# Optimization experiments

Hardware: AMD Instinct MI355X
Metric: run time of the kernel (lower is better)

Reference implementation:

```python
import jax, jax.numpy as jnp
import numpy as np

D = 512
VOCAB = 8192
UTT_LEN = 16
BATCH = 32
NTYPES = 8
MPT = 32
NLAYERS = 2


def setup_inputs() -> dict:
    key = jax.random.key(0)
    ks = jax.random.split(key, 16)
    d, dff, v1 = D, 4 * D, VOCAB + 1
    s = 0.02
    nrm = lambda k, shape: jax.random.normal(k, shape, dtype=jnp.float32) * s
    zeros = lambda shape: jnp.zeros(shape, jnp.float32)
    ones = lambda shape: jnp.ones(shape, jnp.float32)
    return {
        'meanings': jax.random.randint(ks[0], (BATCH, NTYPES), 0, MPT),
        'emb_table': nrm(ks[1], (NTYPES * MPT, d)),
        'v2e_w': nrm(ks[2], (v1, d)),
        'e2v_w': nrm(ks[3], (v1, d)),
        'e2v_b': zeros((v1,)),
        'sa_qkv_w': nrm(ks[4], (NLAYERS, 3 * d, d)),
        'sa_qkv_b': zeros((NLAYERS, 3 * d)),
        'sa_out_w': nrm(ks[5], (NLAYERS, d, d)),
        'sa_out_b': zeros((NLAYERS, d)),
        'ca_qkv_w': nrm(ks[6], (NLAYERS, 3 * d, d)),
        'ca_qkv_b': zeros((NLAYERS, 3 * d)),
        'ca_out_w': nrm(ks[7], (NLAYERS, d, d)),
        'ca_out_b': zeros((NLAYERS, d)),
        'ffn_w1': nrm(ks[8], (NLAYERS, dff, d)),
        'ffn_b1': zeros((NLAYERS, dff)),
        'ffn_w2': nrm(ks[9], (NLAYERS, d, dff)),
        'ffn_b2': zeros((NLAYERS, d)),
        'ln1_g': ones((NLAYERS, d)), 'ln1_b': zeros((NLAYERS, d)),
        'ln2_g': ones((NLAYERS, d)), 'ln2_b': zeros((NLAYERS, d)),
        'ln3_g': ones((NLAYERS, d)), 'ln3_b': zeros((NLAYERS, d)),
    }


def _ln(x, g, b, eps=1e-5):
    m = x.mean(-1, keepdims=True)
    v = ((x - m) ** 2).mean(-1, keepdims=True)
    return (x - m) / jnp.sqrt(v + eps) * g + b


def _attn(q_in, kv_in, qkv_w, qkv_b, out_w, out_b, mask):
    # single-head attention, torch MultiheadAttention layout (seq, batch, d)
    d = q_in.shape[-1]
    q = q_in @ qkv_w[:d].T + qkv_b[:d]
    k = kv_in @ qkv_w[d:2 * d].T + qkv_b[d:2 * d]
    v = kv_in @ qkv_w[2 * d:].T + qkv_b[2 * d:]
    scores = jnp.einsum('qbd,kbd->bqk', q, k) / jnp.sqrt(jnp.float32(d))
    if mask is not None:
        scores = scores + mask
    a = jax.nn.softmax(scores, axis=-1)
    o = jnp.einsum('bqk,kbd->qbd', a, v)
    return o @ out_w.T + out_b


def _sinusoidal_pe(L, d):
    pos = np.arange(L)[:, None].astype(np.float32)
    div = np.exp(np.arange(0, d, 2).astype(np.float32) * (-np.log(10000.0) / d))
    pe = np.zeros((L, d), np.float32)
    pe[:, 0::2] = np.sin(pos * div)
    pe[:, 1::2] = np.cos(pos * div)
    return jnp.asarray(pe)[:, None, :]  # [L,1,d]


def reference(meanings, emb_table, v2e_w, e2v_w, e2v_b,
              sa_qkv_w, sa_qkv_b, sa_out_w, sa_out_b,
              ca_qkv_w, ca_qkv_b, ca_out_w, ca_out_b,
              ffn_w1, ffn_b1, ffn_w2, ffn_b2,
              ln1_g, ln1_b, ln2_g, ln2_b, ln3_g, ln3_b):
    B, T = meanings.shape
    v1, d = v2e_w.shape
    start_token = v1 - 1
    mpt = emb_table.shape[0] // T
    offs = jnp.arange(T, dtype=meanings.dtype) * mpt
    src = emb_table[meanings + offs].sum(axis=1)[None]  # [1,B,d] cross-attn memory
    L = UTT_LEN
    pe = _sinusoidal_pe(L, d)
    causal = jnp.where(jnp.tril(jnp.ones((L, L), bool)), 0.0, -jnp.inf).astype(jnp.float32)
    nlayers = sa_qkv_w.shape[0]

    def step(buf, i):
        # full-length decode with causal mask == original growing-prefix decode at position i
        x = v2e_w[buf[:L]] + pe  # [L,B,d]
        for l in range(nlayers):
            sa = _attn(x, x, sa_qkv_w[l], sa_qkv_b[l], sa_out_w[l], sa_out_b[l], causal)
            x = _ln(x + sa, ln1_g[l], ln1_b[l])
            ca = _attn(x, src, ca_qkv_w[l], ca_qkv_b[l], ca_out_w[l], ca_out_b[l], None)
            x = _ln(x + ca, ln2_g[l], ln2_b[l])
            ff = jax.nn.relu(x @ ffn_w1[l].T + ffn_b1[l]) @ ffn_w2[l].T + ffn_b2[l]
            x = _ln(x + ff, ln3_g[l], ln3_b[l])
        h = jnp.take(x, i, axis=0)         # [B,d] last generated position
        logits = h @ e2v_w.T + e2v_b        # [B,V+1]
        tok = jnp.argmax(logits, axis=-1).astype(buf.dtype)
        buf = buf.at[i + 1].set(tok)
        return buf, (tok, logits)

    buf0 = jnp.zeros((L + 1, B), jnp.int32).at[0].set(start_token)
    _, (toks, logits) = jax.lax.scan(step, buf0, jnp.arange(L))
    return toks, logits  # utterances [utt_len,B], per-step logits [utt_len,B,V+1]
```

## Files before the change

kernel.cpp:

```cpp
#include <hip/hip_runtime.h>
#include <cmath>

namespace {

constexpr int Dm  = 512;
constexpr int Bn  = 32;
constexpr int Lq  = 16;
constexpr int V1  = 8193;
constexpr int DFF = 2048;
constexpr int NL  = 2;
constexpr int NT  = 256;

__device__ __forceinline__ float wred(float v) {
#pragma unroll
  for (int off = 32; off; off >>= 1) v += __shfl_down(v, off, 64);
  return v;
}

__device__ __forceinline__ float dot4(const float4 w, const float4 x, float a) {
  a = fmaf(w.x, x.x, a); a = fmaf(w.y, x.y, a);
  a = fmaf(w.z, x.z, a); a = fmaf(w.w, x.w, a);
  return a;
}

__device__ __forceinline__ float pe_val(int pos, int t) {
  const int j2 = (t >> 1) << 1;
  const float div = expf((float)j2 * (-9.210340371976184f / 512.0f));
  const float ang = (float)pos * div;
  return (t & 1) ? cosf(ang) : sinf(ang);
}

template <int KS, int Kc, int SP, bool RELU>
__global__ __launch_bounds__(NT) void fg_part(
    const float* __restrict__ xsrc, int xstride, int srcPartStride,
    const float* __restrict__ W, int K,
    const float* __restrict__ bias,
    float* __restrict__ part, int N) {
  constexpr int QR = Kc / 4;
  __shared__ float smem[32 * Kc];
  const int kc = (int)blockIdx.x % KS;
  const int k0 = kc * Kc;
  for (int idx = threadIdx.x; idx < 8 * Kc; idx += NT) {
    const int b = idx / QR, q = idx - b * QR;
    const float* s0 = xsrc + (size_t)b * xstride + k0 + (q << 2);
    float4 v = *(const float4*)(s0);
#pragma unroll
    for (int s = 1; s < SP; ++s) {
      const float4 u = *(const float4*)(s0 + (size_t)s * srcPartStride);
      v.x += u.x; v.y += u.y; v.z += u.z; v.w += u.w;
    }
    if (RELU) {
      v.x = fmaxf(v.x, 0.f); v.y = fmaxf(v.y, 0.f);
      v.z = fmaxf(v.z, 0.f); v.w = fmaxf(v.w, 0.f);
    }
    *(float4*)(smem + b * Kc + ((q ^ (b & 7)) << 2)) = v;
  }
  __syncthreads();
  const int lane = (int)threadIdx.x & 63, wave = (int)threadIdx.x >> 6;
  const int bl = lane & 31, nh = lane >> 5, sw = bl & 7;
  const int rowjob = ((int)blockIdx.x / KS) * 4 + wave;
  const int n0 = (rowjob << 3) + (nh << 2);
  const float* xb = smem + bl * Kc;
  const float* w = W + (size_t)n0 * K + k0;
  float a0 = 0.f, a1 = 0.f, a2 = 0.f, a3 = 0.f;
#pragma unroll 4
  for (int qq = 0; qq < QR; ++qq) {
    const float4 xv = *(const float4*)(xb + ((qq ^ sw) << 2));
    const float* wq = w + (qq << 2);
    a0 = dot4(*(const float4*)(wq), xv, a0);
    a1 = dot4(*(const float4*)(wq + K), xv, a1);
    a2 = dot4(*(const float4*)(wq + 2 * K), xv, a2);
    a3 = dot4(*(const float4*)(wq + 3 * K), xv, a3);
  }
  if (kc == 0) {
    a0 += bias[n0]; a1 += bias[n0 + 1]; a2 += bias[n0 + 2]; a3 += bias[n0 + 3];
  }
  float* yb = part + (size_t)kc * 32 * N + (size_t)bl * N + n0;
  yb[0] = a0; yb[1] = a1; yb[2] = a2; yb[3] = a3;
}

__global__ __launch_bounds__(NT) void fg_qkv_part(const float* __restrict__ x,
    const float* __restrict__ W, const float* __restrict__ bias,
    float* __restrict__ qkvp) {
  constexpr int Kc = 128, QR = 32;
  __shared__ float smem[32 * Kc];
  const int kc = (int)blockIdx.x & 3;
  const int k0 = kc * Kc;
  for (int idx = threadIdx.x; idx < 8 * Kc; idx += NT) {
    const int b = idx / QR, q = idx - b * QR;
    const float4 v = *(const float4*)(x + (b << 9) + k0 + (q << 2));
    *(float4*)(smem + b * Kc + ((q ^ (b & 7)) << 2)) = v;
  }
  __syncthreads();
  const int lane = (int)threadIdx.x & 63, wave = (int)threadIdx.x >> 6;
  const int bl = lane & 31, nh = lane >> 5, sw = bl & 7;
  const int rowjob = ((int)blockIdx.x >> 2) * 4 + wave;
  const int n0 = (rowjob << 3) + (nh << 2);
  const float* xb = smem + bl * Kc;
  const float* w = W + (size_t)n0 * Dm + k0;
  float a0 = 0.f, a1 = 0.f, a2 = 0.f, a3 = 0.f;
#pragma unroll 4
  for (int qq = 0; qq < QR; ++qq) {
    const float4 xv = *(const float4*)(xb + ((qq ^ sw) << 2));
    const float* wq = w + (qq << 2);
    a0 = dot4(*(const float4*)(wq), xv, a0);
    a1 = dot4(*(const float4*)(wq + Dm), xv, a1);
    a2 = dot4(*(const float4*)(wq + 2 * Dm), xv, a2);
    a3 = dot4(*(const float4*)(wq + 3 * Dm), xv, a3);
  }
  if (kc == 0) {
    a0 += bias[n0]; a1 += bias[n0 + 1]; a2 += bias[n0 + 2]; a3 += bias[n0 + 3];
  }
  const int seg = n0 >> 9;
  float* yb = qkvp + (size_t)seg * 65536 + (size_t)kc * 16384 + (bl << 9) + (n0 & 511);
  yb[0] = a0; yb[1] = a1; yb[2] = a2; yb[3] = a3;
}

__device__ __forceinline__ void block_ln(float* s, const float* __restrict__ g,
                                         const float* __restrict__ bb, float* red) {
  const int tid = (int)threadIdx.x;
  float ls = 0.f, lq = 0.f;
  for (int t = tid; t < Dm; t += NT) { const float v = s[t]; ls += v; lq += v * v; }
  ls = wred(ls); lq = wred(lq);
  const int wave = tid >> 6, lane = tid & 63;
  if (lane == 0) { red[wave] = ls; red[4 + wave] = lq; }
  __syncthreads();
  const float sum = red[0] + red[1] + red[2] + red[3];
  const float sq  = red[4] + red[5] + red[6] + red[7];
  const float mean = sum * (1.f / Dm);
  const float var  = sq * (1.f / Dm) - mean * mean;
  const float inv  = 1.f / sqrtf(var + 1e-5f);
  __syncthreads();
  for (int t = tid; t < Dm; t += NT) s[t] = (s[t] - mean) * inv * g[t] + bb[t];
}

__global__ __launch_bounds__(NT) void attn_core(const float* __restrict__ qkvp,
    float* __restrict__ kcl, float* __restrict__ vcl,
    float* __restrict__ aout, int pos) {
  __shared__ float sQ[Dm], sK[Dm], sV[Dm], sS[Lq];
  const int b = blockIdx.x, tid = threadIdx.x, lane = tid & 63, wave = tid >> 6;
  const float* qp = qkvp;
  const float* kp = qkvp + 65536;
  const float* vp = qkvp + 131072;
  for (int t = tid; t < Dm; t += NT) {
    const int o = (b << 9) + t;
    const float qv = qp[o] + qp[o + 16384] + qp[o + 32768] + qp[o + 49152];
    const float kv = kp[o] + kp[o + 16384] + kp[o + 32768] + kp[o + 49152];
    const float vv = vp[o] + vp[o + 16384] + vp[o + 32768] + vp[o + 49152];
    sQ[t] = qv; sK[t] = kv; sV[t] = vv;
    const int co = ((pos * Bn + b) << 9) + t;
    kcl[co] = kv; vcl[co] = vv;
  }
  __syncthreads();
  for (int j = wave; j <= pos; j += 4) {
    float acc;
    if (j == pos) {
      acc = dot4(*(const float4*)(sK + (lane << 2)),
                 *(const float4*)(sQ + (lane << 2)), 0.f);
      acc = dot4(*(const float4*)(sK + 256 + (lane << 2)),
                 *(const float4*)(sQ + 256 + (lane << 2)), acc);
    } else {
      const float* kr = kcl + ((size_t)(j * Bn + b) << 9);
      acc = dot4(*(const float4*)(kr + (lane << 2)),
                 *(const float4*)(sQ + (lane << 2)), 0.f);
      acc = dot4(*(const float4*)(kr + 256 + (lane << 2)),
                 *(const float4*)(sQ + 256 + (lane << 2)), acc);
    }
    acc = wred(acc);
    if (lane == 0) sS[j] = acc * 0.044194173824159216f;
  }
  __syncthreads();
  if (tid == 0) {
    float m = -1e30f;
    for (int j = 0; j <= pos; ++j) m = fmaxf(m, sS[j]);
    float s = 0.f;
    for (int j = 0; j <= pos; ++j) { const float e = expf(sS[j] - m); sS[j] = e; s += e; }
    const float inv = 1.f / s;
    for (int j = 0; j <= pos; ++j) sS[j] *= inv;
  }
  __syncthreads();
  for (int t = tid; t < Dm; t += NT) {
    float acc = sS[pos] * sV[t];
    for (int j = 0; j < pos; ++j) acc += sS[j] * vcl[((size_t)(j * Bn + b) << 9) + t];
    aout[(b << 9) + t] = acc;
  }
}

__global__ __launch_bounds__(NT) void ln12(const float* __restrict__ sop,
    const float* __restrict__ caCp,
    const float* __restrict__ g1, const float* __restrict__ b1,
    const float* __restrict__ g2, const float* __restrict__ b2,
    float* __restrict__ x) {
  __shared__ float sR[Dm], red[8];
  const int b = blockIdx.x, tid = threadIdx.x;
  for (int t = tid; t < Dm; t += NT) {
    const int o = (b << 9) + t;
    sR[t] = x[o] + sop[o] + sop[o + 16384] + sop[o + 32768] + sop[o + 49152];
  }
  __syncthreads();
  block_ln(sR, g1, b1, red);
  __syncthreads();
  for (int t = tid; t < Dm; t += NT) {
    const int o = (b << 9) + t;
    sR[t] += caCp[o] + caCp[o + 16384] + caCp[o + 32768] + caCp[o + 49152];
  }
  __syncthreads();
  block_ln(sR, g2, b2, red);
  __syncthreads();
  for (int t = tid; t < Dm; t += NT) x[(b << 9) + t] = sR[t];
}

__global__ __launch_bounds__(NT) void ln3red(const float* __restrict__ f2p,
    const float* __restrict__ g3, const float* __restrict__ bb3,
    float* __restrict__ x) {
  __shared__ float sR[Dm], red[8];
  const int b = blockIdx.x, tid = threadIdx.x;
  for (int t = tid; t < Dm; t += NT) {
    const int o = (b << 9) + t;
    float v = x[o];
#pragma unroll
    for (int kc = 0; kc < 8; ++kc) v += f2p[kc * 16384 + o];
    sR[t] = v;
  }
  __syncthreads();
  block_ln(sR, g3, bb3, red);
  __syncthreads();
  for (int t = tid; t < Dm; t += NT) x[(b << 9) + t] = sR[t];
}

__global__ __launch_bounds__(512) void src_kernel(const int* __restrict__ meanings,
                                                  const float* __restrict__ emb,
                                                  float* __restrict__ src) {
  const int b = blockIdx.x, t = threadIdx.x;
  float s = 0.f;
#pragma unroll
  for (int ty = 0; ty < 8; ++ty) {
    const int idx = meanings[b * 8 + ty] + ty * 32;
    s += emb[(size_t)idx * Dm + t];
  }
  src[b * Dm + t] = s;
}

__global__ __launch_bounds__(512) void embed0(const float* __restrict__ v2e,
                                              float* __restrict__ x) {
  const int b = blockIdx.x, t = threadIdx.x;
  x[(b << 9) + t] = v2e[(size_t)(V1 - 1) * Dm + t] + pe_val(0, t);
}

__global__ __launch_bounds__(NT) void argmax_embed(float* __restrict__ x,
    const float* __restrict__ e2v_w, const float* __restrict__ e2v_b,
    const float* __restrict__ v2e, const float* __restrict__ lp,
    float* __restrict__ outLogits, float* __restrict__ outToks, int i) {
  __shared__ float red[8];
  __shared__ float sv[NT];
  __shared__ int   si[NT];
  const int b = blockIdx.x, tid = threadIdx.x, lane = tid & 63, wave = tid >> 6;
  float ls = 0.f;
  for (int t = tid; t < Dm; t += NT) ls += x[(b << 9) + t] * e2v_w[(size_t)8192 * Dm + t];
  ls = wred(ls);
  if (lane == 0) red[wave] = ls;
  __syncthreads();
  float* row = outLogits + ((size_t)i * Bn + b) * V1;
  if (tid == 0) {
    const float lg = red[0] + red[1] + red[2] + red[3] + e2v_b[8192];
    row[8192] = lg;
    red[4] = lg;
  }
  __syncthreads();
  const float lg = red[4];
  float best = -1e30f; int bi = 0;
  for (int v = tid; v < 8192; v += NT) {
    const float val = lp[(b << 13) + v] + lp[262144 + (b << 13) + v];
    row[v] = val;
    if (val > best) { best = val; bi = v; }
  }
  sv[tid] = best; si[tid] = bi;
  __syncthreads();
  for (int off = 128; off; off >>= 1) {
    if (tid < off) {
      const float v2 = sv[tid + off]; const int i2 = si[tid + off];
      if (v2 > sv[tid] || (v2 == sv[tid] && i2 < si[tid])) { sv[tid] = v2; si[tid] = i2; }
    }
    __syncthreads();
  }
  if (tid == 0) {
    int tok = si[0];
    if (lg > sv[0]) tok = 8192;
    outToks[i * Bn + b] = (float)tok;
    si[0] = tok;
  }
  __syncthreads();
  const int tok = si[0];
  if (i + 1 < Lq) {
    for (int t = tid; t < Dm; t += NT)
      x[(b << 9) + t] = v2e[(size_t)tok * Dm + t] + pe_val(i + 1, t);
  }
}

}

extern "C" void kernel_launch(void* const* d_in, const int* in_sizes, int n_in,
                              void* d_out, int out_size, void* d_ws, size_t ws_size,
                              hipStream_t stream) {
  (void)in_sizes; (void)n_in; (void)out_size; (void)ws_size;
  const int*   meanings  = (const int*)d_in[0];
  const float* emb_table = (const float*)d_in[1];
  const float* v2e_w     = (const float*)d_in[2];
  const float* e2v_w     = (const float*)d_in[3];
  const float* e2v_b     = (const float*)d_in[4];
  const float* sa_qkv_w  = (const float*)d_in[5];
  const float* sa_qkv_b  = (const float*)d_in[6];
  const float* sa_out_w  = (const float*)d_in[7];
  const float* sa_out_b  = (const float*)d_in[8];
  const float* ca_qkv_w  = (const float*)d_in[9];
  const float* ca_qkv_b  = (const float*)d_in[10];
  const float* ca_out_w  = (const float*)d_in[11];
  const float* ca_out_b  = (const float*)d_in[12];
  const float* ffn_w1    = (const float*)d_in[13];
  const float* ffn_b1    = (const float*)d_in[14];
  const float* ffn_w2    = (const float*)d_in[15];
  const float* ffn_b2    = (const float*)d_in[16];
  const float* ln1_g     = (const float*)d_in[17];
  const float* ln1_b     = (const float*)d_in[18];
  const float* ln2_g     = (const float*)d_in[19];
  const float* ln2_b     = (const float*)d_in[20];
  const float* ln3_g     = (const float*)d_in[21];
  const float* ln3_b     = (const float*)d_in[22];

  float* out = (float*)d_out;
  float* outLogits = out + Lq * Bn;

  float* f = (float*)d_ws;
  float* src  = f;  f += 16384;
  float* x    = f;  f += 16384;
  float* aout = f;  f += 16384;
  float* caCp = f;  f += 131072;
  float* regA = f;  f += 655360;
  float* kcache = f; f += 524288;
  float* vcache = f;
  float* qkvp = regA;
  float* sop  = regA + 196608;
  float* h1p  = regA + 262144;
  float* f2p  = regA + 524288;
  float* lp   = regA;

  src_kernel<<<Bn, 512, 0, stream>>>(meanings, emb_table, src);

  for (int l = 0; l < NL; ++l) {
    fg_part<4, 128, 1, false><<<64, NT, 0, stream>>>(src, Dm, 0,
        ca_qkv_w + ((size_t)l * 3 + 2) * Dm * Dm, Dm,
        ca_qkv_b + l * 3 * Dm + 2 * Dm, sop, Dm);
    fg_part<4, 128, 4, false><<<64, NT, 0, stream>>>(sop, Dm, 16384,
        ca_out_w + (size_t)l * Dm * Dm, Dm,
        ca_out_b + l * Dm, caCp + (size_t)l * 65536, Dm);
  }

  embed0<<<Bn, 512, 0, stream>>>(v2e_w, x);

  for (int i = 0; i < Lq; ++i) {
    for (int l = 0; l < NL; ++l) {
      float* kcl = kcache + (size_t)l * Lq * Bn * Dm;
      float* vcl = vcache + (size_t)l * Lq * Bn * Dm;
      fg_qkv_part<<<192, NT, 0, stream>>>(x,
          sa_qkv_w + (size_t)l * 3 * Dm * Dm, sa_qkv_b + l * 3 * Dm, qkvp);
      attn_core<<<Bn, NT, 0, stream>>>(qkvp, kcl, vcl, aout, i);
      fg_part<4, 128, 1, false><<<64, NT, 0, stream>>>(aout, Dm, 0,
          sa_out_w + (size_t)l * Dm * Dm, Dm, sa_out_b + l * Dm, sop, Dm);
      ln12<<<Bn, NT, 0, stream>>>(sop, caCp + (size_t)l * 65536,
          ln1_g + l * Dm, ln1_b + l * Dm, ln2_g + l * Dm, ln2_b + l * Dm, x);
      fg_part<4, 128, 1, false><<<256, NT, 0, stream>>>(x, Dm, 0,
          ffn_w1 + (size_t)l * DFF * Dm, Dm, ffn_b1 + l * DFF, h1p, DFF);
      fg_part<8, 256, 4, true><<<128, NT, 0, stream>>>(h1p, DFF, 65536,
          ffn_w2 + (size_t)l * Dm * DFF, DFF, ffn_b2 + l * Dm, f2p, Dm);
      ln3red<<<Bn, NT, 0, stream>>>(f2p,
          ln3_g + l * Dm, ln3_b + l * Dm, x);
    }
    fg_part<2, 256, 1, false><<<512, NT, 0, stream>>>(x, Dm, 0,
        e2v_w, Dm, e2v_b, lp, 8192);
    argmax_embed<<<Bn, NT, 0, stream>>>(x, e2v_w, e2v_b, v2e_w,
        lp, outLogits, out, i);
  }
}
```

Measured before the change: 2.736 ms.

## Fuse decode-step kernels using atomic ticket counters and in-kernel grid waits

Merges the per-layer chain of GEMV, attention, layernorm and FFN kernels into three kernels per step (qkv+attention, post-attention+FFN, logits+argmax). Global atomic counters act as barriers: the last-arriving blocks take tickets to run the dependent reduction or attention stages, and other blocks spin-wait on counters between phases. The aim is to cut kernel launch count and launch gaps in a latency-bound decode loop. In exchange, global traffic now uses relaxed atomic loads and stores, which may be slower than plain vector loads. The spin waits also assume every block is co-resident on the GPU, which holds for grids of up to 256 blocks.

```diff
diff --git a/kernel.cpp b/kernel.cpp
--- a/kernel.cpp
+++ b/kernel.cpp
@@ -11,6 +11,27 @@
 constexpr int NL  = 2;
 constexpr int NT  = 256;
 
+__device__ __forceinline__ float g_ld(const float* p) {
+  return __hip_atomic_load(p, __ATOMIC_RELAXED, __HIP_MEMORY_SCOPE_AGENT);
+}
+__device__ __forceinline__ void g_st(float* p, float v) {
+  __hip_atomic_store(p, v, __ATOMIC_RELAXED, __HIP_MEMORY_SCOPE_AGENT);
+}
+__device__ __forceinline__ float2 g_ld2(const float* p) {
+  unsigned long long u = __hip_atomic_load((const unsigned long long*)p,
+      __ATOMIC_RELAXED, __HIP_MEMORY_SCOPE_AGENT);
+  float2 r;
+  r.x = __uint_as_float((unsigned)u);
+  r.y = __uint_as_float((unsigned)(u >> 32));
+  return r;
+}
+__device__ __forceinline__ void g_st2(float* p, float a, float b) {
+  unsigned long long u = (unsigned long long)__float_as_uint(a) |
+                         ((unsigned long long)__float_as_uint(b) << 32);
+  __hip_atomic_store((unsigned long long*)p, u, __ATOMIC_RELAXED,
+                     __HIP_MEMORY_SCOPE_AGENT);
+}
+
 __device__ __forceinline__ float wred(float v) {
 #pragma unroll
   for (int off = 32; off; off >>= 1) v += __shfl_down(v, off, 64);
@@ -30,37 +51,87 @@
   return (t & 1) ? cosf(ang) : sinf(ang);
 }
 
+__device__ __forceinline__ void wait_ctr(const unsigned* c, unsigned n) {
+  if (threadIdx.x == 0) {
+    while (__hip_atomic_load(c, __ATOMIC_RELAXED, __HIP_MEMORY_SCOPE_AGENT) < n)
+      __builtin_amdgcn_s_sleep(2);
+    asm volatile("" ::: "memory");
+  }
+  __syncthreads();
+}
+
+__device__ void block_ln(float* s, const float* __restrict__ g,
+                         const float* __restrict__ bb, float* red) {
+  const int tid = (int)threadIdx.x;
+  float ls = 0.f, lq = 0.f;
+  for (int t = tid; t < Dm; t += NT) { const float v = s[t]; ls += v; lq += v * v; }
+  ls = wred(ls); lq = wred(lq);
+  const int wave = tid >> 6, lane = tid & 63;
+  if (lane == 0) { red[wave] = ls; red[4 + wave] = lq; }
+  __syncthreads();
+  const float sum = red[0] + red[1] + red[2] + red[3];
+  const float sq  = red[4] + red[5] + red[6] + red[7];
+  const float mean = sum * (1.f / Dm);
+  const float var  = sq * (1.f / Dm) - mean * mean;
+  const float inv  = 1.f / sqrtf(var + 1e-5f);
+  __syncthreads();
+  for (int t = tid; t < Dm; t += NT) s[t] = (s[t] - mean) * inv * g[t] + bb[t];
+}
+
+__global__ __launch_bounds__(512) void init_bar(unsigned* bar) {
+  const int i = (int)blockIdx.x * 512 + (int)threadIdx.x;
+  __hip_atomic_store(bar + i, 0u, __ATOMIC_RELAXED, __HIP_MEMORY_SCOPE_AGENT);
+}
+
+__global__ __launch_bounds__(512) void src_kernel(const int* __restrict__ meanings,
+    const float* __restrict__ emb, float* __restrict__ src) {
+  const int b = (int)blockIdx.x, t = (int)threadIdx.x;
+  float s = 0.f;
+#pragma unroll
+  for (int ty = 0; ty < 8; ++ty) {
+    const int idx = meanings[b * 8 + ty] + ty * 32;
+    s += emb[(size_t)idx * Dm + t];
+  }
+  g_st(src + b * Dm + t, s);
+}
+
+__global__ __launch_bounds__(512) void embed0(const float* __restrict__ v2e,
+                                              float* __restrict__ x) {
+  const int b = (int)blockIdx.x, t = (int)threadIdx.x;
+  g_st(x + (b << 9) + t, v2e[(size_t)(V1 - 1) * Dm + t] + pe_val(0, t));
+}
+
 template <int KS, int Kc, int SP, bool RELU>
-__global__ __launch_bounds__(NT) void fg_part(
-    const float* __restrict__ xsrc, int xstride, int srcPartStride,
-    const float* __restrict__ W, int K,
-    const float* __restrict__ bias,
+__global__ __launch_bounds__(NT) void k_fg(const float* __restrict__ xsrc, int xstride,
+    int pstride, const float* __restrict__ W, int K, const float* __restrict__ bias,
     float* __restrict__ part, int N) {
   constexpr int QR = Kc / 4;
   __shared__ float smem[32 * Kc];
-  const int kc = (int)blockIdx.x % KS;
-  const int k0 = kc * Kc;
-  for (int idx = threadIdx.x; idx < 8 * Kc; idx += NT) {
+  const int bid = (int)blockIdx.x, tid = (int)threadIdx.x;
+  const int kc = bid % KS, k0 = kc * Kc;
+  for (int idx = tid; idx < 8 * Kc; idx += NT) {
     const int b = idx / QR, q = idx - b * QR;
     const float* s0 = xsrc + (size_t)b * xstride + k0 + (q << 2);
-    float4 v = *(const float4*)(s0);
+    float2 lo = g_ld2(s0), hi = g_ld2(s0 + 2);
 #pragma unroll
     for (int s = 1; s < SP; ++s) {
-      const float4 u = *(const float4*)(s0 + (size_t)s * srcPartStride);
-      v.x += u.x; v.y += u.y; v.z += u.z; v.w += u.w;
+      const float2 l2 = g_ld2(s0 + (size_t)s * pstride);
+      const float2 h2 = g_ld2(s0 + (size_t)s * pstride + 2);
+      lo.x += l2.x; lo.y += l2.y; hi.x += h2.x; hi.y += h2.y;
     }
     if (RELU) {
-      v.x = fmaxf(v.x, 0.f); v.y = fmaxf(v.y, 0.f);
-      v.z = fmaxf(v.z, 0.f); v.w = fmaxf(v.w, 0.f);
-    }
+      lo.x = fmaxf(lo.x, 0.f); lo.y = fmaxf(lo.y, 0.f);
+      hi.x = fmaxf(hi.x, 0.f); hi.y = fmaxf(hi.y, 0.f);
+    }
+    float4 v; v.x = lo.x; v.y = lo.y; v.z = hi.x; v.w = hi.y;
     *(float4*)(smem + b * Kc + ((q ^ (b & 7)) << 2)) = v;
   }
   __syncthreads();
-  const int lane = (int)threadIdx.x & 63, wave = (int)threadIdx.x >> 6;
+  const int lane = tid & 63, wave = tid >> 6;
   const int bl = lane & 31, nh = lane >> 5, sw = bl & 7;
-  const int rowjob = ((int)blockIdx.x / KS) * 4 + wave;
+  const float* xb = smem + bl * Kc;
+  const int rowjob = (bid / KS) * 4 + wave;
   const int n0 = (rowjob << 3) + (nh << 2);
-  const float* xb = smem + bl * Kc;
   const float* w = W + (size_t)n0 * K + k0;
   float a0 = 0.f, a1 = 0.f, a2 = 0.f, a3 = 0.f;
 #pragma unroll 4
@@ -76,77 +147,68 @@
     a0 += bias[n0]; a1 += bias[n0 + 1]; a2 += bias[n0 + 2]; a3 += bias[n0 + 3];
   }
   float* yb = part + (size_t)kc * 32 * N + (size_t)bl * N + n0;
-  yb[0] = a0; yb[1] = a1; yb[2] = a2; yb[3] = a3;
-}
-
-__global__ __launch_bounds__(NT) void fg_qkv_part(const float* __restrict__ x,
+  g_st2(yb, a0, a1); g_st2(yb + 2, a2, a3);
+}
+
+__global__ __launch_bounds__(NT) void k_qkv_attn(const float* __restrict__ x,
     const float* __restrict__ W, const float* __restrict__ bias,
-    float* __restrict__ qkvp) {
-  constexpr int Kc = 128, QR = 32;
-  __shared__ float smem[32 * Kc];
-  const int kc = (int)blockIdx.x & 3;
-  const int k0 = kc * Kc;
-  for (int idx = threadIdx.x; idx < 8 * Kc; idx += NT) {
-    const int b = idx / QR, q = idx - b * QR;
-    const float4 v = *(const float4*)(x + (b << 9) + k0 + (q << 2));
-    *(float4*)(smem + b * Kc + ((q ^ (b & 7)) << 2)) = v;
-  }
-  __syncthreads();
-  const int lane = (int)threadIdx.x & 63, wave = (int)threadIdx.x >> 6;
-  const int bl = lane & 31, nh = lane >> 5, sw = bl & 7;
-  const int rowjob = ((int)blockIdx.x >> 2) * 4 + wave;
-  const int n0 = (rowjob << 3) + (nh << 2);
-  const float* xb = smem + bl * Kc;
-  const float* w = W + (size_t)n0 * Dm + k0;
-  float a0 = 0.f, a1 = 0.f, a2 = 0.f, a3 = 0.f;
+    float* __restrict__ qkvp, float* __restrict__ kcl, float* __restrict__ vcl,
+    float* __restrict__ aout, unsigned* ctr, int pos) {
+  __shared__ float smem[4096];
+  __shared__ int tkt_s;
+  const int bid = (int)blockIdx.x, tid = (int)threadIdx.x;
+  const int lane = tid & 63, wave = tid >> 6;
+  {
+    constexpr int Kc = 128;
+    const int kc = bid & 3, k0 = kc << 7;
+    for (int idx = tid; idx < 1024; idx += NT) {
+      const int b = idx >> 5, q = idx & 31;
+      const float* s0 = x + (b << 9) + k0 + (q << 2);
+      const float2 lo = g_ld2(s0), hi = g_ld2(s0 + 2);
+      float4 v; v.x = lo.x; v.y = lo.y; v.z = hi.x; v.w = hi.y;
+      *(float4*)(smem + b * Kc + ((q ^ (b & 7)) << 2)) = v;
+    }
+    __syncthreads();
+    const int bl = lane & 31, nh = lane >> 5, sw = bl & 7;
+    const float* xb = smem + bl * Kc;
+    const int rowjob = (bid >> 2) * 4 + wave;
+    const int n0 = (rowjob << 3) + (nh << 2);
+    const float* w = W + (size_t)n0 * Dm + k0;
+    float a0 = 0.f, a1 = 0.f, a2 = 0.f, a3 = 0.f;
 #pragma unroll 4
-  for (int qq = 0; qq < QR; ++qq) {
-    const float4 xv = *(const float4*)(xb + ((qq ^ sw) << 2));
-    const float* wq = w + (qq << 2);
-    a0 = dot4(*(const float4*)(wq), xv, a0);
-    a1 = dot4(*(const float4*)(wq + Dm), xv, a1);
-    a2 = dot4(*(const float4*)(wq + 2 * Dm), xv, a2);
-    a3 = dot4(*(const float4*)(wq + 3 * Dm), xv, a3);
-  }
-  if (kc == 0) {
-    a0 += bias[n0]; a1 += bias[n0 + 1]; a2 += bias[n0 + 2]; a3 += bias[n0 + 3];
-  }
-  const int seg = n0 >> 9;
-  float* yb = qkvp + (size_t)seg * 65536 + (size_t)kc * 16384 + (bl << 9) + (n0 & 511);
-  yb[0] = a0; yb[1] = a1; yb[2] = a2; yb[3] = a3;
-}
-
-__device__ __forceinline__ void block_ln(float* s, const float* __restrict__ g,
-                                         const float* __restrict__ bb, float* red) {
-  const int tid = (int)threadIdx.x;
-  float ls = 0.f, lq = 0.f;
-  for (int t = tid; t < Dm; t += NT) { const float v = s[t]; ls += v; lq += v * v; }
-  ls = wred(ls); lq = wred(lq);
-  const int wave = tid >> 6, lane = tid & 63;
-  if (lane == 0) { red[wave] = ls; red[4 + wave] = lq; }
-  __syncthreads();
-  const float sum = red[0] + red[1] + red[2] + red[3];
-  const float sq  = red[4] + red[5] + red[6] + red[7];
-  const float mean = sum * (1.f / Dm);
-  const float var  = sq * (1.f / Dm) - mean * mean;
-  const float inv  = 1.f / sqrtf(var + 1e-5f);
-  __syncthreads();
-  for (int t = tid; t < Dm; t += NT) s[t] = (s[t] - mean) * inv * g[t] + bb[t];
-}
-
-__global__ __launch_bounds__(NT) void attn_core(const float* __restrict__ qkvp,
-    float* __restrict__ kcl, float* __restrict__ vcl,
-    float* __restrict__ aout, int pos) {
-  __shared__ float sQ[Dm], sK[Dm], sV[Dm], sS[Lq];
-  const int b = blockIdx.x, tid = threadIdx.x, lane = tid & 63, wave = tid >> 6;
+    for (int qq = 0; qq < 32; ++qq) {
+      const float4 xv = *(const float4*)(xb + ((qq ^ sw) << 2));
+      const float* wq = w + (qq << 2);
+      a0 = dot4(*(const float4*)(wq), xv, a0);
+      a1 = dot4(*(const float4*)(wq + Dm), xv, a1);
+      a2 = dot4(*(const float4*)(wq + 2 * Dm), xv, a2);
+      a3 = dot4(*(const float4*)(wq + 3 * Dm), xv, a3);
+    }
+    if (kc == 0) {
+      a0 += bias[n0]; a1 += bias[n0 + 1]; a2 += bias[n0 + 2]; a3 += bias[n0 + 3];
+    }
+    const int seg = n0 >> 9;
+    float* yb = qkvp + (size_t)seg * 65536 + (size_t)kc * 16384 + (bl << 9) + (n0 & 511);
+    g_st2(yb, a0, a1); g_st2(yb + 2, a2, a3);
+  }
+  __syncthreads();
+  if (tid == 0)
+    tkt_s = (int)__hip_atomic_fetch_add(ctr, 1u, __ATOMIC_RELEASE, __HIP_MEMORY_SCOPE_AGENT);
+  __syncthreads();
+  const int tkt = tkt_s;
+  if (tkt < 160) return;
+  const int b = tkt - 160;
+  wait_ctr(ctr, 192);
+  float* sQ = smem; float* sK = smem + 512; float* sV = smem + 1024;
+  float* sS = smem + 1536;
   const float* qp = qkvp;
   const float* kp = qkvp + 65536;
   const float* vp = qkvp + 131072;
   for (int t = tid; t < Dm; t += NT) {
     const int o = (b << 9) + t;
-    const float qv = qp[o] + qp[o + 16384] + qp[o + 32768] + qp[o + 49152];
-    const float kv = kp[o] + kp[o + 16384] + kp[o + 32768] + kp[o + 49152];
-    const float vv = vp[o] + vp[o + 16384] + vp[o + 32768] + vp[o + 49152];
+    const float qv = g_ld(qp + o) + g_ld(qp + o + 16384) + g_ld(qp + o + 32768) + g_ld(qp + o + 49152);
+    const float kv = g_ld(kp + o) + g_ld(kp + o + 16384) + g_ld(kp + o + 32768) + g_ld(kp + o + 49152);
+    const float vv = g_ld(vp + o) + g_ld(vp + o + 16384) + g_ld(vp + o + 32768) + g_ld(vp + o + 49152);
     sQ[t] = qv; sK[t] = kv; sV[t] = vv;
     const int co = ((pos * Bn + b) << 9) + t;
     kcl[co] = kv; vcl[co] = vv;
@@ -182,97 +244,266 @@
   for (int t = tid; t < Dm; t += NT) {
     float acc = sS[pos] * sV[t];
     for (int j = 0; j < pos; ++j) acc += sS[j] * vcl[((size_t)(j * Bn + b) << 9) + t];
-    aout[(b << 9) + t] = acc;
-  }
-}
-
-__global__ __launch_bounds__(NT) void ln12(const float* __restrict__ sop,
-    const float* __restrict__ caCp,
+    g_st(aout + (b << 9) + t, acc);
+  }
+}
+
+__global__ __launch_bounds__(NT) void k_post(
+    const float* __restrict__ aout, const float* __restrict__ caCp_l,
+    float* __restrict__ x,
+    const float* __restrict__ saW, const float* __restrict__ saB,
     const float* __restrict__ g1, const float* __restrict__ b1,
     const float* __restrict__ g2, const float* __restrict__ b2,
-    float* __restrict__ x) {
-  __shared__ float sR[Dm], red[8];
-  const int b = blockIdx.x, tid = threadIdx.x;
-  for (int t = tid; t < Dm; t += NT) {
-    const int o = (b << 9) + t;
-    sR[t] = x[o] + sop[o] + sop[o + 16384] + sop[o + 32768] + sop[o + 49152];
-  }
-  __syncthreads();
-  block_ln(sR, g1, b1, red);
-  __syncthreads();
-  for (int t = tid; t < Dm; t += NT) {
-    const int o = (b << 9) + t;
-    sR[t] += caCp[o] + caCp[o + 16384] + caCp[o + 32768] + caCp[o + 49152];
-  }
-  __syncthreads();
-  block_ln(sR, g2, b2, red);
-  __syncthreads();
-  for (int t = tid; t < Dm; t += NT) x[(b << 9) + t] = sR[t];
-}
-
-__global__ __launch_bounds__(NT) void ln3red(const float* __restrict__ f2p,
-    const float* __restrict__ g3, const float* __restrict__ bb3,
-    float* __restrict__ x) {
-  __shared__ float sR[Dm], red[8];
-  const int b = blockIdx.x, tid = threadIdx.x;
-  for (int t = tid; t < Dm; t += NT) {
-    const int o = (b << 9) + t;
-    float v = x[o];
+    const float* __restrict__ f1W, const float* __restrict__ f1b,
+    const float* __restrict__ f2W, const float* __restrict__ f2b,
+    const float* __restrict__ g3, const float* __restrict__ b3,
+    float* __restrict__ sop, float* __restrict__ h1p, float* __restrict__ f2p,
+    unsigned* ctr) {
+  __shared__ float smem[8192];
+  __shared__ float red_s[8];
+  __shared__ int tkt_s;
+  const int bid = (int)blockIdx.x, tid = (int)threadIdx.x;
+  const int lane = tid & 63, wave = tid >> 6;
+  const int bl = lane & 31, nh = lane >> 5, sw = bl & 7;
+  unsigned* c0 = ctr; unsigned* c1 = ctr + 32; unsigned* c2 = ctr + 64;
+  unsigned* c3 = ctr + 96;
+
+  if (bid < 64) {
+    const int kc = bid & 3, k0 = kc << 7;
+    for (int idx = tid; idx < 1024; idx += NT) {
+      const int b = idx >> 5, q = idx & 31;
+      const float* s0 = aout + (b << 9) + k0 + (q << 2);
+      const float2 lo = g_ld2(s0), hi = g_ld2(s0 + 2);
+      float4 v; v.x = lo.x; v.y = lo.y; v.z = hi.x; v.w = hi.y;
+      *(float4*)(smem + (b << 7) + ((q ^ (b & 7)) << 2)) = v;
+    }
+    __syncthreads();
+    const float* xb = smem + (bl << 7);
+    const int rowjob = (bid >> 2) * 4 + wave;
+    const int n0 = (rowjob << 3) + (nh << 2);
+    const float* w = saW + (size_t)n0 * Dm + k0;
+    float a0 = 0.f, a1 = 0.f, a2 = 0.f, a3 = 0.f;
+#pragma unroll 4
+    for (int qq = 0; qq < 32; ++qq) {
+      const float4 xv = *(const float4*)(xb + ((qq ^ sw) << 2));
+      const float* wq = w + (qq << 2);
+      a0 = dot4(*(const float4*)(wq), xv, a0);
+      a1 = dot4(*(const float4*)(wq + Dm), xv, a1);
+      a2 = dot4(*(const float4*)(wq + 2 * Dm), xv, a2);
+      a3 = dot4(*(const float4*)(wq + 3 * Dm), xv, a3);
+    }
+    if (kc == 0) {
+      a0 += saB[n0]; a1 += saB[n0 + 1]; a2 += saB[n0 + 2]; a3 += saB[n0 + 3];
+    }
+    float* yb = sop + (size_t)kc * 16384 + (bl << 9) + n0;
+    g_st2(yb, a0, a1); g_st2(yb + 2, a2, a3);
+    __syncthreads();
+    if (tid == 0)
+      tkt_s = (int)__hip_atomic_fetch_add(c0, 1u, __ATOMIC_RELEASE, __HIP_MEMORY_SCOPE_AGENT);
+    __syncthreads();
+    const int tkt = tkt_s;
+    if (tkt >= 32) {
+      const int b = tkt - 32;
+      wait_ctr(c0, 64);
+      float* sR = smem;
+      for (int t = tid; t < Dm; t += NT) {
+        const int o = (b << 9) + t;
+        sR[t] = g_ld(x + o) + g_ld(sop + o) + g_ld(sop + o + 16384) +
+                g_ld(sop + o + 32768) + g_ld(sop + o + 49152);
+      }
+      __syncthreads();
+      block_ln(sR, g1, b1, red_s);
+      __syncthreads();
+      for (int t = tid; t < Dm; t += NT) {
+        const int o = (b << 9) + t;
+        sR[t] += g_ld(caCp_l + o) + g_ld(caCp_l + o + 16384) +
+                 g_ld(caCp_l + o + 32768) + g_ld(caCp_l + o + 49152);
+      }
+      __syncthreads();
+      block_ln(sR, g2, b2, red_s);
+      __syncthreads();
+      for (int t = tid; t < Dm; t += NT) g_st(x + (b << 9) + t, sR[t]);
+      __syncthreads();
+      if (tid == 0)
+        __hip_atomic_fetch_add(c1, 1u, __ATOMIC_RELEASE, __HIP_MEMORY_SCOPE_AGENT);
+    }
+  }
+
+  wait_ctr(c1, 32);
+
+  {
+    const int kc = bid & 3, k0 = kc << 7;
+    for (int idx = tid; idx < 1024; idx += NT) {
+      const int b = idx >> 5, q = idx & 31;
+      const float* s0 = x + (b << 9) + k0 + (q << 2);
+      const float2 lo = g_ld2(s0), hi = g_ld2(s0 + 2);
+      float4 v; v.x = lo.x; v.y = lo.y; v.z = hi.x; v.w = hi.y;
+      *(float4*)(smem + (b << 7) + ((q ^ (b & 7)) << 2)) = v;
+    }
+    __syncthreads();
+    const float* xb = smem + (bl << 7);
+    const int rowjob = (bid >> 2) * 4 + wave;
+    const int n0 = (rowjob << 3) + (nh << 2);
+    const float* w = f1W + (size_t)n0 * Dm + k0;
+    float a0 = 0.f, a1 = 0.f, a2 = 0.f, a3 = 0.f;
+#pragma unroll 4
+    for (int qq = 0; qq < 32; ++qq) {
+      const float4 xv = *(const float4*)(xb + ((qq ^ sw) << 2));
+      const float* wq = w + (qq << 2);
+      a0 = dot4(*(const float4*)(wq), xv, a0);
+      a1 = dot4(*(const float4*)(wq + Dm), xv, a1);
+      a2 = dot4(*(const float4*)(wq + 2 * Dm), xv, a2);
+      a3 = dot4(*(const float4*)(wq + 3 * Dm), xv, a3);
+    }
+    if (kc == 0) {
+      a0 += f1b[n0]; a1 += f1b[n0 + 1]; a2 += f1b[n0 + 2]; a3 += f1b[n0 + 3];
+    }
+    float* yb = h1p + (size_t)kc * 65536 + (size_t)bl * DFF + n0;
+    g_st2(yb, a0, a1); g_st2(yb + 2, a2, a3);
+  }
+  __syncthreads();
+  if (tid == 0)
+    __hip_atomic_fetch_add(c2, 1u, __ATOMIC_RELEASE, __HIP_MEMORY_SCOPE_AGENT);
+  if (bid >= 128) return;
+
+  wait_ctr(c2, 256);
+
+  {
+    const int kc = bid & 7, k0 = kc << 8;
+    for (int idx = tid; idx < 2048; idx += NT) {
+      const int b = idx >> 6, q = idx & 63;
+      const float* s0 = h1p + (size_t)b * DFF + k0 + (q << 2);
+      float2 lo = g_ld2(s0), hi = g_ld2(s0 + 2);
 #pragma unroll
-    for (int kc = 0; kc < 8; ++kc) v += f2p[kc * 16384 + o];
-    sR[t] = v;
-  }
-  __syncthreads();
-  block_ln(sR, g3, bb3, red);
-  __syncthreads();
-  for (int t = tid; t < Dm; t += NT) x[(b << 9) + t] = sR[t];
-}
-
-__global__ __launch_bounds__(512) void src_kernel(const int* __restrict__ meanings,
-                                                  const float* __restrict__ emb,
-                                                  float* __restrict__ src) {
-  const int b = blockIdx.x, t = threadIdx.x;
-  float s = 0.f;
+      for (int s = 1; s < 4; ++s) {
+        const float2 l2 = g_ld2(s0 + (size_t)s * 65536);
+        const float2 h2 = g_ld2(s0 + (size_t)s * 65536 + 2);
+        lo.x += l2.x; lo.y += l2.y; hi.x += h2.x; hi.y += h2.y;
+      }
+      lo.x = fmaxf(lo.x, 0.f); lo.y = fmaxf(lo.y, 0.f);
+      hi.x = fmaxf(hi.x, 0.f); hi.y = fmaxf(hi.y, 0.f);
+      float4 v; v.x = lo.x; v.y = lo.y; v.z = hi.x; v.w = hi.y;
+      *(float4*)(smem + (b << 8) + ((q ^ (b & 7)) << 2)) = v;
+    }
+    __syncthreads();
+    const float* xb = smem + (bl << 8);
+    const int rowjob = (bid >> 3) * 4 + wave;
+    const int n0 = (rowjob << 3) + (nh << 2);
+    const float* w = f2W + (size_t)n0 * DFF + k0;
+    float a0 = 0.f, a1 = 0.f, a2 = 0.f, a3 = 0.f;
+#pragma unroll 4
+    for (int qq = 0; qq < 64; ++qq) {
+      const float4 xv = *(const float4*)(xb + ((qq ^ sw) << 2));
+      const float* wq = w + (qq << 2);
+      a0 = dot4(*(const float4*)(wq), xv, a0);
+      a1 = dot4(*(const float4*)(wq + DFF), xv, a1);
+      a2 = dot4(*(const float4*)(wq + 2 * DFF), xv, a2);
+      a3 = dot4(*(const float4*)(wq + 3 * DFF), xv, a3);
+    }
+    if (kc == 0) {
+      a0 += f2b[n0]; a1 += f2b[n0 + 1]; a2 += f2b[n0 + 2]; a3 += f2b[n0 + 3];
+    }
+    float* yb = f2p + (size_t)kc * 16384 + (bl << 9) + n0;
+    g_st2(yb, a0, a1); g_st2(yb + 2, a2, a3);
+  }
+  __syncthreads();
+  if (tid == 0)
+    tkt_s = (int)__hip_atomic_fetch_add(c3, 1u, __ATOMIC_RELEASE, __HIP_MEMORY_SCOPE_AGENT);
+  __syncthreads();
+  const int tkt = tkt_s;
+  if (tkt < 96) return;
+  const int b = tkt - 96;
+  wait_ctr(c3, 128);
+  {
+    float* sR = smem;
+    for (int t = tid; t < Dm; t += NT) {
+      const int o = (b << 9) + t;
+      float v = g_ld(x + o);
 #pragma unroll
-  for (int ty = 0; ty < 8; ++ty) {
-    const int idx = meanings[b * 8 + ty] + ty * 32;
-    s += emb[(size_t)idx * Dm + t];
-  }
-  src[b * Dm + t] = s;
-}
-
-__global__ __launch_bounds__(512) void embed0(const float* __restrict__ v2e,
-                                              float* __restrict__ x) {
-  const int b = blockIdx.x, t = threadIdx.x;
-  x[(b << 9) + t] = v2e[(size_t)(V1 - 1) * Dm + t] + pe_val(0, t);
-}
-
-__global__ __launch_bounds__(NT) void argmax_embed(float* __restrict__ x,
+      for (int kc = 0; kc < 8; ++kc) v += g_ld(f2p + kc * 16384 + o);
+      sR[t] = v;
+    }
+    __syncthreads();
+    block_ln(sR, g3, b3, red_s);
+    __syncthreads();
+    for (int t = tid; t < Dm; t += NT) g_st(x + (b << 9) + t, sR[t]);
+  }
+}
+
+__global__ __launch_bounds__(NT) void k_logits(float* __restrict__ x,
     const float* __restrict__ e2v_w, const float* __restrict__ e2v_b,
-    const float* __restrict__ v2e, const float* __restrict__ lp,
-    float* __restrict__ outLogits, float* __restrict__ outToks, int i) {
-  __shared__ float red[8];
+    const float* __restrict__ v2e, float* __restrict__ lp,
+    float* __restrict__ outLogits, float* __restrict__ outToks,
+    unsigned* ctr, int i) {
+  __shared__ float smem[8192];
+  __shared__ float red_s[8];
+  __shared__ float lg_s;
   __shared__ float sv[NT];
   __shared__ int   si[NT];
-  const int b = blockIdx.x, tid = threadIdx.x, lane = tid & 63, wave = tid >> 6;
+  __shared__ int tkt_s;
+  const int bid = (int)blockIdx.x, tid = (int)threadIdx.x;
+  const int lane = tid & 63, wave = tid >> 6;
+  {
+    const int kc = bid & 1, k0 = kc << 8;
+    for (int idx = tid; idx < 2048; idx += NT) {
+      const int b = idx >> 6, q = idx & 63;
+      const float* s0 = x + (b << 9) + k0 + (q << 2);
+      const float2 lo = g_ld2(s0), hi = g_ld2(s0 + 2);
+      float4 v; v.x = lo.x; v.y = lo.y; v.z = hi.x; v.w = hi.y;
+      *(float4*)(smem + (b << 8) + ((q ^ (b & 7)) << 2)) = v;
+    }
+    __syncthreads();
+    const int bl = lane & 31, nh = lane >> 5, sw = bl & 7;
+    const float* xb = smem + (bl << 8);
+    const int rowjob = (bid >> 1) * 4 + wave;
+    const int n0 = (rowjob << 3) + (nh << 2);
+    const float* w = e2v_w + (size_t)n0 * Dm + k0;
+    float a0 = 0.f, a1 = 0.f, a2 = 0.f, a3 = 0.f;
+#pragma unroll 4
+    for (int qq = 0; qq < 64; ++qq) {
+      const float4 xv = *(const float4*)(xb + ((qq ^ sw) << 2));
+      const float* wq = w + (qq << 2);
+      a0 = dot4(*(const float4*)(wq), xv, a0);
+      a1 = dot4(*(const float4*)(wq + Dm), xv, a1);
+      a2 = dot4(*(const float4*)(wq + 2 * Dm), xv, a2);
+      a3 = dot4(*(const float4*)(wq + 3 * Dm), xv, a3);
+    }
+    if (kc == 0) {
+      a0 += e2v_b[n0]; a1 += e2v_b[n0 + 1]; a2 += e2v_b[n0 + 2]; a3 += e2v_b[n0 + 3];
+    }
+    float* yb = lp + (size_t)kc * 262144 + (size_t)((lane & 31)) * 8192 + n0;
+    g_st2(yb, a0, a1); g_st2(yb + 2, a2, a3);
+  }
+  __syncthreads();
+  if (tid == 0)
+    tkt_s = (int)__hip_atomic_fetch_add(ctr, 1u, __ATOMIC_RELEASE, __HIP_MEMORY_SCOPE_AGENT);
+  __syncthreads();
+  const int tkt = tkt_s;
+  if (tkt < 480) return;
+  const int b = tkt - 480;
+  wait_ctr(ctr, 512);
   float ls = 0.f;
-  for (int t = tid; t < Dm; t += NT) ls += x[(b << 9) + t] * e2v_w[(size_t)8192 * Dm + t];
+  for (int t = tid; t < Dm; t += NT)
+    ls += g_ld(x + (b << 9) + t) * e2v_w[(size_t)8192 * Dm + t];
   ls = wred(ls);
-  if (lane == 0) red[wave] = ls;
+  if (lane == 0) red_s[wave] = ls;
   __syncthreads();
   float* row = outLogits + ((size_t)i * Bn + b) * V1;
   if (tid == 0) {
-    const float lg = red[0] + red[1] + red[2] + red[3] + e2v_b[8192];
+    const float lg = red_s[0] + red_s[1] + red_s[2] + red_s[3] + e2v_b[8192];
     row[8192] = lg;
-    red[4] = lg;
-  }
-  __syncthreads();
-  const float lg = red[4];
+    lg_s = lg;
+  }
+  __syncthreads();
+  const float lg = lg_s;
   float best = -1e30f; int bi = 0;
-  for (int v = tid; v < 8192; v += NT) {
-    const float val = lp[(b << 13) + v] + lp[262144 + (b << 13) + v];
-    row[v] = val;
-    if (val > best) { best = val; bi = v; }
+  for (int v0 = tid * 2; v0 < 8192; v0 += NT * 2) {
+    const float2 a = g_ld2(lp + (b << 13) + v0);
+    const float2 c = g_ld2(lp + 262144 + (b << 13) + v0);
+    const float va = a.x + c.x, vb = a.y + c.y;
+    row[v0] = va; row[v0 + 1] = vb;
+    if (va > best) { best = va; bi = v0; }
+    if (vb > best) { best = vb; bi = v0 + 1; }
   }
   sv[tid] = best; si[tid] = bi;
   __syncthreads();
@@ -293,7 +524,7 @@
   const int tok = si[0];
   if (i + 1 < Lq) {
     for (int t = tid; t < Dm; t += NT)
-      x[(b << 9) + t] = v2e[(size_t)tok * Dm + t] + pe_val(i + 1, t);
+      g_st(x + (b << 9) + t, v2e[(size_t)tok * Dm + t] + pe_val(i + 1, t));
   }
 }
 
@@ -330,7 +561,9 @@
   float* out = (float*)d_out;
   float* outLogits = out + Lq * Bn;
 
-  float* f = (float*)d_ws;
+  char* ws = (char*)d_ws;
+  unsigned* bar = (unsigned*)ws;
+  float* f = (float*)(ws + 32768);
   float* src  = f;  f += 16384;
   float* x    = f;  f += 16384;
   float* aout = f;  f += 16384;
@@ -344,13 +577,16 @@
   float* f2p  = regA + 524288;
   float* lp   = regA;
 
+  int cidx = 0;
+
+  init_bar<<<16, 512, 0, stream>>>(bar);
   src_kernel<<<Bn, 512, 0, stream>>>(meanings, emb_table, src);
 
   for (int l = 0; l < NL; ++l) {
-    fg_part<4, 128, 1, false><<<64, NT, 0, stream>>>(src, Dm, 0,
+    k_fg<4, 128, 1, false><<<64, NT, 0, stream>>>(src, Dm, 0,
         ca_qkv_w + ((size_t)l * 3 + 2) * Dm * Dm, Dm,
         ca_qkv_b + l * 3 * Dm + 2 * Dm, sop, Dm);
-    fg_part<4, 128, 4, false><<<64, NT, 0, stream>>>(sop, Dm, 16384,
+    k_fg<4, 128, 4, false><<<64, NT, 0, stream>>>(sop, Dm, 16384,
         ca_out_w + (size_t)l * Dm * Dm, Dm,
         ca_out_b + l * Dm, caCp + (size_t)l * 65536, Dm);
   }
@@ -361,23 +597,19 @@
     for (int l = 0; l < NL; ++l) {
       float* kcl = kcache + (size_t)l * Lq * Bn * Dm;
       float* vcl = vcache + (size_t)l * Lq * Bn * Dm;
-      fg_qkv_part<<<192, NT, 0, stream>>>(x,
-          sa_qkv_w + (size_t)l * 3 * Dm * Dm, sa_qkv_b + l * 3 * Dm, qkvp);
-      attn_core<<<Bn, NT, 0, stream>>>(qkvp, kcl, vcl, aout, i);
-      fg_part<4, 128, 1, false><<<64, NT, 0, stream>>>(aout, Dm, 0,
-          sa_out_w + (size_t)l * Dm * Dm, Dm, sa_out_b + l * Dm, sop, Dm);
-      ln12<<<Bn, NT, 0, stream>>>(sop, caCp + (size_t)l * 65536,
-          ln1_g + l * Dm, ln1_b + l * Dm, ln2_g + l * Dm, ln2_b + l * Dm, x);
-      fg_part<4, 128, 1, false><<<256, NT, 0, stream>>>(x, Dm, 0,
-          ffn_w1 + (size_t)l * DFF * Dm, Dm, ffn_b1 + l * DFF, h1p, DFF);
-      fg_part<8, 256, 4, true><<<128, NT, 0, stream>>>(h1p, DFF, 65536,
-          ffn_w2 + (size_t)l * Dm * DFF, DFF, ffn_b2 + l * Dm, f2p, Dm);
-      ln3red<<<Bn, NT, 0, stream>>>(f2p,
-          ln3_g + l * Dm, ln3_b + l * Dm, x);
-    }
-    fg_part<2, 256, 1, false><<<512, NT, 0, stream>>>(x, Dm, 0,
-        e2v_w, Dm, e2v_b, lp, 8192);
-    argmax_embed<<<Bn, NT, 0, stream>>>(x, e2v_w, e2v_b, v2e_w,
-        lp, outLogits, out, i);
-  }
-}
+      k_qkv_attn<<<192, NT, 0, stream>>>(x,
+          sa_qkv_w + (size_t)l * 3 * Dm * Dm, sa_qkv_b + l * 3 * Dm,
+          qkvp, kcl, vcl, aout, bar + (cidx++) * 32, i);
+      k_post<<<256, NT, 0, stream>>>(aout, caCp + (size_t)l * 65536, x,
+          sa_out_w + (size_t)l * Dm * Dm, sa_out_b + l * Dm,
+          ln1_g + l * Dm, ln1_b + l * Dm, ln2_g + l * Dm, ln2_b + l * Dm,
+          ffn_w1 + (size_t)l * DFF * Dm, ffn_b1 + l * DFF,
+          ffn_w2 + (size_t)l * Dm * DFF, ffn_b2 + l * Dm,
+          ln3_g + l * Dm, ln3_b + l * Dm,
+          sop, h1p, f2p, bar + cidx * 32);
+      cidx += 4;
+    }
+    k_logits<<<512, NT, 0, stream>>>(x, e2v_w, e2v_b, v2e_w, lp,
+        outLogits, out, bar + (cidx++) * 32, i);
+  }
+}
```

Result: slower. 3.237 ms (+18.3%).
